# Optimization experiments

Hardware: AMD Instinct MI355X
Metric: run time of the kernel (lower is better)

## Reference

```python
import jax, jax.numpy as jnp
import numpy as np

N = 50000   # nodes
E = 800000  # edges (avg degree 16)
F = 128     # feature dim (input = hidden = output)
H = 8       # heads
D = F // H  # head dim = 16
L = 4       # layers


def setup_inputs() -> dict:
    key = jax.random.key(0)
    ks = jax.random.split(key, 11)
    x = jax.random.normal(ks[0], (N, F), dtype=jnp.float32)
    edge_index = jax.random.randint(ks[1], (2, E), 0, N, dtype=jnp.int64)
    s = 1.0 / np.sqrt(F)
    Wq = jax.random.normal(ks[2], (L, F, F), dtype=jnp.float32) * s
    Wk = jax.random.normal(ks[3], (L, F, F), dtype=jnp.float32) * s
    Wv = jax.random.normal(ks[4], (L, F, F), dtype=jnp.float32) * s
    Ws = jax.random.normal(ks[5], (L, F, F), dtype=jnp.float32) * s  # lin_skip (root weight)
    bq = jax.random.normal(ks[6], (L, F), dtype=jnp.float32) * 0.02
    bk = jax.random.normal(ks[7], (L, F), dtype=jnp.float32) * 0.02
    bv = jax.random.normal(ks[8], (L, F), dtype=jnp.float32) * 0.02
    bs = jax.random.normal(ks[9], (L, F), dtype=jnp.float32) * 0.02
    return {"x": x, "edge_index": edge_index, "Wq": Wq, "bq": bq,
            "Wk": Wk, "bk": bk, "Wv": Wv, "bv": bv, "Ws": Ws, "bs": bs}


def _transformer_conv(x, src, dst, Wq, bq, Wk, bk, Wv, bv, Ws, bs):
    # Q from destination nodes, K/V from source nodes (PyG TransformerConv).
    q = (x @ Wq + bq)[dst].reshape(E, H, D)
    k = (x @ Wk + bk)[src].reshape(E, H, D)
    alpha = (q * k).sum(-1) * (1.0 / np.sqrt(D))            # [E, H]
    # segment softmax over edges grouped by destination node
    amax = jax.ops.segment_max(alpha, dst, num_segments=N)   # [N, H]
    amax = jnp.where(jnp.isfinite(amax), amax, 0.0)
    p = jnp.exp(alpha - amax[dst])
    denom = jax.ops.segment_sum(p, dst, num_segments=N)      # [N, H]
    a = p / denom[dst]                                       # [E, H]
    v = (x @ Wv + bv)[src].reshape(E, H, D)
    msg = (a[..., None] * v).reshape(E, F)
    out = jax.ops.segment_sum(msg, dst, num_segments=N)      # concat heads
    out = out + x @ Ws + bs                                  # root/skip connection
    return out, a


def reference(x, edge_index, Wq, bq, Wk, bk, Wv, bv, Ws, bs):
    src, dst = edge_index[0], edge_index[1]
    alphas = []
    h = x
    for i in range(L - 1):
        h, a = _transformer_conv(h, src, dst, Wq[i], bq[i], Wk[i], bk[i],
                                 Wv[i], bv[i], Ws[i], bs[i])
        h = jax.nn.gelu(h, approximate=False)
        alphas.append(a)
    h, a = _transformer_conv(h, src, dst, Wq[-1], bq[-1], Wk[-1], bk[-1],
                             Wv[-1], bv[-1], Ws[-1], bs[-1])
    alphas.append(a)
    return h, jnp.stack(alphas)  # [N, F], [L, E, H]
```

## Files before the change

kernel.cpp:

```cpp
#include <hip/hip_runtime.h>
#include <math.h>

#define F 128
#define HEADS 8

typedef __attribute__((ext_vector_type(8))) short short8;
typedef __attribute__((ext_vector_type(4))) float floatx4;
typedef __attribute__((ext_vector_type(2))) _Float16 half2v;

__device__ __forceinline__ unsigned short f2bf(float f) {
    unsigned u = __float_as_uint(f);
    unsigned r = u + 0x7FFFu + ((u >> 16) & 1u);
    return (unsigned short)(r >> 16);
}

__device__ __forceinline__ half2v ashalf2(unsigned u) {
    return __builtin_bit_cast(half2v, u);
}
__device__ __forceinline__ unsigned pkh(float a, float b) {
    return __builtin_bit_cast(unsigned, __builtin_amdgcn_cvt_pkrtz(a, b));
}

#if __has_builtin(__builtin_amdgcn_fdot2)
#define FDOT2(a, b, c) __builtin_amdgcn_fdot2((a), (b), (c), false)
#else
#define FDOT2(a, b, c) ((c) + (float)(a)[0] * (float)(b)[0] + (float)(a)[1] * (float)(b)[1])
#endif


__global__ __launch_bounds__(256) void hist_k(const int* __restrict__ dst, int E, int* __restrict__ deg) {
    int e = blockIdx.x * 256 + threadIdx.x;
    if (e < E) atomicAdd(&deg[dst[e]], 1);
}

__global__ __launch_bounds__(256) void scan1_k(const int* __restrict__ deg, int N,
                                               int* __restrict__ start, int* __restrict__ partials) {
    __shared__ int sm[256];
    int t = threadIdx.x;
    int i = blockIdx.x * 256 + t;
    int v = (i < N) ? deg[i] : 0;
    sm[t] = v;
    __syncthreads();
    for (int off = 1; off < 256; off <<= 1) {
        int add = (t >= off) ? sm[t - off] : 0;
        __syncthreads();
        sm[t] += add;
        __syncthreads();
    }
    if (i < N) start[i] = sm[t] - v;
    if (t == 255) partials[blockIdx.x] = sm[t];
}

__global__ __launch_bounds__(256) void scan2_k(int* __restrict__ partials, int nb,
                                               int* __restrict__ start, int N, int E) {
    __shared__ int sm[256];
    int t = threadIdx.x;
    int v = (t < nb) ? partials[t] : 0;
    sm[t] = v;
    __syncthreads();
    for (int off = 1; off < 256; off <<= 1) {
        int add = (t >= off) ? sm[t - off] : 0;
        __syncthreads();
        sm[t] += add;
        __syncthreads();
    }
    if (t < nb) partials[t] = sm[t] - v;
    if (t == 0) start[N] = E;
}

__global__ __launch_bounds__(256) void scan3_k(int* __restrict__ start, int N, const int* __restrict__ partials) {
    int i = blockIdx.x * 256 + threadIdx.x;
    if (i < N) start[i] += partials[blockIdx.x];
}

__global__ __launch_bounds__(256) void fill_k(const int* __restrict__ src, const int* __restrict__ dst, int E,
                                              const int* __restrict__ start, int* __restrict__ cursor,
                                              int2* __restrict__ epair) {
    int e = blockIdx.x * 256 + threadIdx.x;
    if (e < E) {
        int dd = dst[e];
        int pos = atomicAdd(&cursor[dd], 1);
        epair[start[dd] + pos] = make_int2(e, src[e]);
    }
}

__global__ __launch_bounds__(256) void cvt_k(const float* __restrict__ x, unsigned short* __restrict__ xb, int total4) {
    int i = blockIdx.x * 256 + threadIdx.x;
    if (i < total4) {
        float4 v = ((const float4*)x)[i];
        ushort4 o;
        o.x = f2bf(v.x); o.y = f2bf(v.y); o.z = f2bf(v.z); o.w = f2bf(v.w);
        ((ushort4*)xb)[i] = o;
    }
}


__global__ __launch_bounds__(256) void wprep_k(
    const float* __restrict__ Wq, const float* __restrict__ Wk,
    const float* __restrict__ Wv, const float* __restrict__ Ws,
    unsigned short* __restrict__ out, int total) {
    int idx = blockIdx.x * 256 + threadIdx.x;
    if (idx >= total) return;
    int j = idx & 7;
    int lane = (idx >> 3) & 63;
    int rest = idx >> 9;
    int chunk = rest & 3;
    int ftile = (rest >> 2) & 7;
    int mat = (rest >> 5) & 3;
    int layer = rest >> 7;
    int k = chunk * 32 + (lane >> 4) * 8 + j;
    int f = ftile * 16 + (lane & 15);
    const float* W = (mat == 0) ? Wq : (mat == 1) ? Wk : (mat == 2) ? Wv : Ws;
    out[idx] = f2bf(W[((size_t)layer * F + k) * F + f]);
}


__global__ __launch_bounds__(256) void gemm_mfma(
    const unsigned short* __restrict__ xb, const unsigned short* __restrict__ wfrag,
    const float* __restrict__ bq, const float* __restrict__ bk,
    const float* __restrict__ bv, const float* __restrict__ bs,
    unsigned short* __restrict__ Qh, unsigned short* __restrict__ Kh,
    unsigned short* __restrict__ Vh, float* __restrict__ S, int N) {
    int wave = threadIdx.x >> 6;
    int lane = threadIdx.x & 63;
    int row0 = blockIdx.x * 32;
    int lm = lane & 15, quad = lane >> 4;
    const unsigned short* wf = wfrag + wave * 16384;

    floatx4 acc[2][8];
#pragma unroll
    for (int t = 0; t < 2; t++)
#pragma unroll
        for (int u = 0; u < 8; u++) acc[t][u] = (floatx4){0.f, 0.f, 0.f, 0.f};

#pragma unroll
    for (int chunk = 0; chunk < 4; chunk++) {
        short8 xfr[2];
#pragma unroll
        for (int t = 0; t < 2; t++) {
            int m = row0 + t * 16 + lm;
            m = (m < N) ? m : (N - 1);
            xfr[t] = *(const short8*)(xb + (size_t)m * F + chunk * 32 + quad * 8);
        }
#pragma unroll
        for (int u = 0; u < 8; u++) {
            short8 wfr = *(const short8*)(wf + ((u * 4 + chunk) * 64 + lane) * 8);
            acc[0][u] = __builtin_amdgcn_mfma_f32_16x16x32_bf16(wfr, xfr[0], acc[0][u], 0, 0, 0);
            acc[1][u] = __builtin_amdgcn_mfma_f32_16x16x32_bf16(wfr, xfr[1], acc[1][u], 0, 0, 0);
        }
    }

    const float* bias = (wave == 0) ? bq : (wave == 1) ? bk : (wave == 2) ? bv : bs;
#pragma unroll
    for (int u = 0; u < 8; u++) {
        float4 bv4 = *(const float4*)&bias[u * 16 + quad * 4];
#pragma unroll
        for (int t = 0; t < 2; t++) {
            int node = row0 + t * 16 + lm;
            if (node < N) {
                floatx4 a = acc[t][u];
                size_t off = (size_t)node * F + u * 16 + quad * 4;
                float v0 = a[0] + bv4.x, v1 = a[1] + bv4.y, v2 = a[2] + bv4.z, v3 = a[3] + bv4.w;
                if (wave == 3) {
                    *(float4*)&S[off] = make_float4(v0, v1, v2, v3);
                } else {
                    unsigned short* dp = (wave == 0) ? Qh : (wave == 1) ? Kh : Vh;
                    *(uint2*)&dp[off] = make_uint2(pkh(v0, v1), pkh(v2, v3));
                }
            }
        }
    }
}


__device__ __forceinline__ float gelu_exact(float v) {
    return 0.5f * v * (1.0f + erff(v * 0.70710678118654752f));
}

__global__ __launch_bounds__(256) void edge_k(
    const unsigned short* __restrict__ Qh, const unsigned short* __restrict__ Kh,
    const unsigned short* __restrict__ Vh, const float* __restrict__ S,
    const int* __restrict__ start, const int2* __restrict__ epair,
    float* __restrict__ aout,
    float* __restrict__ hout_f, unsigned short* __restrict__ hout_b,
    int N, int do_gelu) {
    __shared__ float wbuf[4][64][8];
    __shared__ int sbuf[4][64];
    __shared__ int ebuf[4][64];
    __shared__ float mdbuf[4][8];

    int wv = threadIdx.x >> 6;
    int lane = threadIdx.x & 63;
    int n = blockIdx.x * 4 + wv;
    if (n >= N) return;

    int beg = start[n], end = start[n + 1];
    int deg = end - beg;
    bool multi = deg > 64;
    int slot = lane >> 3, h = lane & 7;
    int g = lane >> 4, fl = lane & 15;
    int fh = fl >> 1;

    const unsigned short* qp = Qh + (size_t)n * F + h * 16;
    uint4 qa = *(const uint4*)(qp);
    uint4 qc = *(const uint4*)(qp + 8);
    half2v q0 = ashalf2(qa.x), q1 = ashalf2(qa.y), q2 = ashalf2(qa.z), q3 = ashalf2(qa.w);
    half2v q4 = ashalf2(qc.x), q5 = ashalf2(qc.y), q6 = ashalf2(qc.z), q7 = ashalf2(qc.w);

    float d = 0.f;
    float a0 = 0.f, a1 = 0.f, a2 = 0.f, a3 = 0.f, a4 = 0.f, a5 = 0.f, a6 = 0.f, a7 = 0.f;

    for (int c0 = beg; c0 < end; c0 += 64) {
        int cnt = min(64, end - c0);

        int nit = (cnt + 7) >> 3;
        for (int it = 0; it < nit; it++) {
            int idx = it * 8 + slot;
            bool val = idx < cnt;
            int gi = c0 + (val ? idx : 0);
            int2 pe = epair[gi];
            int s = pe.y;
            const unsigned short* kp = Kh + (size_t)s * F + h * 16;
            uint4 ka = *(const uint4*)(kp);
            uint4 kc = *(const uint4*)(kp + 8);
            float p0 = 0.f, p1 = 0.f;
            p0 = FDOT2(q0, ashalf2(ka.x), p0);
            p0 = FDOT2(q1, ashalf2(ka.y), p0);
            p0 = FDOT2(q2, ashalf2(ka.z), p0);
            p0 = FDOT2(q3, ashalf2(ka.w), p0);
            p1 = FDOT2(q4, ashalf2(kc.x), p1);
            p1 = FDOT2(q5, ashalf2(kc.y), p1);
            p1 = FDOT2(q6, ashalf2(kc.z), p1);
            p1 = FDOT2(q7, ashalf2(kc.w), p1);
            float w = __expf((p0 + p1) * 0.25f);
            if (!val) w = 0.f;
            d += w;
            wbuf[wv][idx][h] = w;
            if (h == 0) { sbuf[wv][idx] = s; ebuf[wv][idx] = pe.x; }
            if (multi && val) aout[(size_t)pe.x * HEADS + h] = w;
        }

        for (int j = 0; j < cnt; j += 8) {
            int idx0 = j + g;
            int idx1 = j + 4 + g;
            bool v0 = idx0 < cnt;
            bool v1 = idx1 < cnt;
            int s0 = sbuf[wv][v0 ? idx0 : 0];
            int s1 = sbuf[wv][v1 ? idx1 : 0];
            float w0 = wbuf[wv][v0 ? idx0 : 0][fh];
            float w1 = wbuf[wv][v1 ? idx1 : 0][fh];
            if (!v0) w0 = 0.f;
            if (!v1) w1 = 0.f;
            uint4 va = *(const uint4*)&Vh[(size_t)s0 * F + fl * 8];
            uint4 vb2 = *(const uint4*)&Vh[(size_t)s1 * F + fl * 8];
            half2v x0 = ashalf2(va.x), x1 = ashalf2(va.y), x2 = ashalf2(va.z), x3 = ashalf2(va.w);
            half2v y0 = ashalf2(vb2.x), y1 = ashalf2(vb2.y), y2 = ashalf2(vb2.z), y3 = ashalf2(vb2.w);
            a0 += w0 * (float)x0[0]; a1 += w0 * (float)x0[1];
            a2 += w0 * (float)x1[0]; a3 += w0 * (float)x1[1];
            a4 += w0 * (float)x2[0]; a5 += w0 * (float)x2[1];
            a6 += w0 * (float)x3[0]; a7 += w0 * (float)x3[1];
            a0 += w1 * (float)y0[0]; a1 += w1 * (float)y0[1];
            a2 += w1 * (float)y1[0]; a3 += w1 * (float)y1[1];
            a4 += w1 * (float)y2[0]; a5 += w1 * (float)y2[1];
            a6 += w1 * (float)y3[0]; a7 += w1 * (float)y3[1];
        }
    }

    d += __shfl_xor(d, 8);
    d += __shfl_xor(d, 16);
    d += __shfl_xor(d, 32);
    float inv_d = (d > 0.f) ? 1.f / d : 0.f;
    if (slot == 0) mdbuf[wv][h] = inv_d;

    if (!multi) {
        for (int idx = slot; idx < deg; idx += 8)
            aout[(size_t)ebuf[wv][idx] * HEADS + h] = wbuf[wv][idx][h] * inv_d;
    } else {
        for (int idx = slot; idx < deg; idx += 8)
            aout[(size_t)epair[beg + idx].x * HEADS + h] *= inv_d;
    }

    a0 += __shfl_xor(a0, 16); a0 += __shfl_xor(a0, 32);
    a1 += __shfl_xor(a1, 16); a1 += __shfl_xor(a1, 32);
    a2 += __shfl_xor(a2, 16); a2 += __shfl_xor(a2, 32);
    a3 += __shfl_xor(a3, 16); a3 += __shfl_xor(a3, 32);
    a4 += __shfl_xor(a4, 16); a4 += __shfl_xor(a4, 32);
    a5 += __shfl_xor(a5, 16); a5 += __shfl_xor(a5, 32);
    a6 += __shfl_xor(a6, 16); a6 += __shfl_xor(a6, 32);
    a7 += __shfl_xor(a7, 16); a7 += __shfl_xor(a7, 32);

    if (lane < 16) {
        float invd = mdbuf[wv][fh];
        const float* sp = S + (size_t)n * F + fl * 8;
        float4 s0 = *(const float4*)(sp + 0);
        float4 s1 = *(const float4*)(sp + 4);
        float o0 = a0 * invd + s0.x, o1 = a1 * invd + s0.y;
        float o2 = a2 * invd + s0.z, o3 = a3 * invd + s0.w;
        float o4 = a4 * invd + s1.x, o5 = a5 * invd + s1.y;
        float o6 = a6 * invd + s1.z, o7 = a7 * invd + s1.w;
        if (do_gelu) {
            o0 = gelu_exact(o0); o1 = gelu_exact(o1); o2 = gelu_exact(o2); o3 = gelu_exact(o3);
            o4 = gelu_exact(o4); o5 = gelu_exact(o5); o6 = gelu_exact(o6); o7 = gelu_exact(o7);
            uint4 ob;
            ob.x = (unsigned)f2bf(o0) | ((unsigned)f2bf(o1) << 16);
            ob.y = (unsigned)f2bf(o2) | ((unsigned)f2bf(o3) << 16);
            ob.z = (unsigned)f2bf(o4) | ((unsigned)f2bf(o5) << 16);
            ob.w = (unsigned)f2bf(o6) | ((unsigned)f2bf(o7) << 16);
            *(uint4*)&hout_b[(size_t)n * F + fl * 8] = ob;
        } else {
            float* op = hout_f + (size_t)n * F + fl * 8;
            *(float4*)(op + 0) = make_float4(o0, o1, o2, o3);
            *(float4*)(op + 4) = make_float4(o4, o5, o6, o7);
        }
    }
}


extern "C" void kernel_launch(void* const* d_in, const int* in_sizes, int n_in,
                              void* d_out, int out_size, void* d_ws, size_t ws_size,
                              hipStream_t stream) {
    const float* x  = (const float*)d_in[0];
    const int*   ei = (const int*)d_in[1];
    const float* Wq = (const float*)d_in[2];
    const float* bq = (const float*)d_in[3];
    const float* Wk = (const float*)d_in[4];
    const float* bk = (const float*)d_in[5];
    const float* Wv = (const float*)d_in[6];
    const float* bv = (const float*)d_in[7];
    const float* Ws = (const float*)d_in[8];
    const float* bs = (const float*)d_in[9];

    const int N = in_sizes[0] / F;
    const int E = in_sizes[1] / 2;
    const int L = in_sizes[2] / (F * F);

    float* Sb = (float*)d_ws;
    unsigned short* Qh = (unsigned short*)(Sb + (size_t)N * F);
    unsigned short* xb = Qh + (size_t)N * F;
    unsigned short* hb = xb + (size_t)N * F;
    unsigned short* Kb = hb + (size_t)N * F;
    unsigned short* Vb = Kb + (size_t)N * F;
    unsigned short* wfrag = Vb + (size_t)N * F;
    int2* epair = (int2*)(wfrag + (size_t)L * 4 * 16384);
    int* start = (int*)(epair + E);
    int* cursor = start + (N + 1);
    int* partials = cursor + N;

    float* out_h = (float*)d_out;
    float* out_a = out_h + (size_t)N * F;

    const int* srcIdx = ei;
    const int* dstIdx = ei + E;

    int nbScan = (N + 255) / 256;
    hipMemsetAsync(cursor, 0, sizeof(int) * N, stream);
    hist_k<<<(E + 255) / 256, 256, 0, stream>>>(dstIdx, E, cursor);
    scan1_k<<<nbScan, 256, 0, stream>>>(cursor, N, start, partials);
    scan2_k<<<1, 256, 0, stream>>>(partials, nbScan, start, N, E);
    scan3_k<<<nbScan, 256, 0, stream>>>(start, N, partials);
    hipMemsetAsync(cursor, 0, sizeof(int) * N, stream);
    fill_k<<<(E + 255) / 256, 256, 0, stream>>>(srcIdx, dstIdx, E, start, cursor, epair);

    int wtotal = L * 4 * 16384;
    wprep_k<<<(wtotal + 255) / 256, 256, 0, stream>>>(Wq, Wk, Wv, Ws, wfrag, wtotal);
    cvt_k<<<((N * F / 4) + 255) / 256, 256, 0, stream>>>(x, xb, N * F / 4);

    for (int l = 0; l < L; ++l) {
        const unsigned short* hin = (l == 0) ? xb : hb;
        gemm_mfma<<<(N + 31) / 32, 256, 0, stream>>>(
            hin, wfrag + (size_t)l * 4 * 16384,
            bq + (size_t)l * F, bk + (size_t)l * F,
            bv + (size_t)l * F, bs + (size_t)l * F,
            Qh, Kb, Vb, Sb, N);
        edge_k<<<(N + 3) / 4, 256, 0, stream>>>(
            Qh, Kb, Vb, Sb, start, epair,
            out_a + (size_t)l * E * HEADS, out_h, hb, N, (l < L - 1) ? 1 : 0);
    }
}
```

Measured before the change: 685.8 us.

## Load edge pairs once per chunk into registers and software-prefetch K/V gathers

Each lane now loads one (edge id, source) pair per 64-edge chunk, and the indices are broadcast with wave shuffles instead of being staged through shared sbuf/ebuf arrays. The K-row gather for the next iteration and the V-row gathers for the next step are issued before the current dot products and accumulations, a register double-buffering scheme meant to hide gather latency. This raises register pressure, and the clamped prefetch indices cause some redundant loads at chunk tails.

```diff
diff --git a/kernel.cpp b/kernel.cpp
--- a/kernel.cpp
+++ b/kernel.cpp
@@ -185,8 +185,6 @@
     float* __restrict__ hout_f, unsigned short* __restrict__ hout_b,
     int N, int do_gelu) {
     __shared__ float wbuf[4][64][8];
-    __shared__ int sbuf[4][64];
-    __shared__ int ebuf[4][64];
     __shared__ float mdbuf[4][8];
 
     int wv = threadIdx.x >> 6;
@@ -209,20 +207,32 @@
 
     float d = 0.f;
     float a0 = 0.f, a1 = 0.f, a2 = 0.f, a3 = 0.f, a4 = 0.f, a5 = 0.f, a6 = 0.f, a7 = 0.f;
+    int2 peL = make_int2(0, 0);
 
     for (int c0 = beg; c0 < end; c0 += 64) {
         int cnt = min(64, end - c0);
 
+        int2 pe = epair[c0 + min(lane, cnt - 1)];
+        peL = pe;
+
+        int s0 = __shfl(pe.y, g, 64);
+        int s1 = __shfl(pe.y, 4 + g, 64);
+        uint4 va = *(const uint4*)&Vh[(size_t)s0 * F + fl * 8];
+        uint4 vb2 = *(const uint4*)&Vh[(size_t)s1 * F + fl * 8];
+
         int nit = (cnt + 7) >> 3;
+        int idx = slot;
+        int s = __shfl(pe.y, idx, 64);
+        const unsigned short* kp = Kh + (size_t)s * F + h * 16;
+        uint4 ka = *(const uint4*)kp;
+        uint4 kc = *(const uint4*)(kp + 8);
         for (int it = 0; it < nit; it++) {
-            int idx = it * 8 + slot;
+            int nidx = idx + 8;
+            int ns = __shfl(pe.y, min(nidx, 63), 64);
+            const unsigned short* nkp = Kh + (size_t)ns * F + h * 16;
+            uint4 nka = *(const uint4*)nkp;
+            uint4 nkc = *(const uint4*)(nkp + 8);
             bool val = idx < cnt;
-            int gi = c0 + (val ? idx : 0);
-            int2 pe = epair[gi];
-            int s = pe.y;
-            const unsigned short* kp = Kh + (size_t)s * F + h * 16;
-            uint4 ka = *(const uint4*)(kp);
-            uint4 kc = *(const uint4*)(kp + 8);
             float p0 = 0.f, p1 = 0.f;
             p0 = FDOT2(q0, ashalf2(ka.x), p0);
             p0 = FDOT2(q1, ashalf2(ka.y), p0);
@@ -236,23 +246,22 @@
             if (!val) w = 0.f;
             d += w;
             wbuf[wv][idx][h] = w;
-            if (h == 0) { sbuf[wv][idx] = s; ebuf[wv][idx] = pe.x; }
-            if (multi && val) aout[(size_t)pe.x * HEADS + h] = w;
+            if (multi) {
+                int eid = __shfl(pe.x, idx, 64);
+                if (val) aout[(size_t)eid * HEADS + h] = w;
+            }
+            ka = nka; kc = nkc; idx = nidx;
         }
 
         for (int j = 0; j < cnt; j += 8) {
-            int idx0 = j + g;
-            int idx1 = j + 4 + g;
-            bool v0 = idx0 < cnt;
-            bool v1 = idx1 < cnt;
-            int s0 = sbuf[wv][v0 ? idx0 : 0];
-            int s1 = sbuf[wv][v1 ? idx1 : 0];
-            float w0 = wbuf[wv][v0 ? idx0 : 0][fh];
-            float w1 = wbuf[wv][v1 ? idx1 : 0][fh];
-            if (!v0) w0 = 0.f;
-            if (!v1) w1 = 0.f;
-            uint4 va = *(const uint4*)&Vh[(size_t)s0 * F + fl * 8];
-            uint4 vb2 = *(const uint4*)&Vh[(size_t)s1 * F + fl * 8];
+            int ns0 = __shfl(pe.y, min(j + 8 + g, 63), 64);
+            int ns1 = __shfl(pe.y, min(j + 12 + g, 63), 64);
+            uint4 na = *(const uint4*)&Vh[(size_t)ns0 * F + fl * 8];
+            uint4 nb = *(const uint4*)&Vh[(size_t)ns1 * F + fl * 8];
+            bool v0 = (j + g) < cnt;
+            bool v1 = (j + 4 + g) < cnt;
+            float w0 = v0 ? wbuf[wv][j + g][fh] : 0.f;
+            float w1 = v1 ? wbuf[wv][j + 4 + g][fh] : 0.f;
             half2v x0 = ashalf2(va.x), x1 = ashalf2(va.y), x2 = ashalf2(va.z), x3 = ashalf2(va.w);
             half2v y0 = ashalf2(vb2.x), y1 = ashalf2(vb2.y), y2 = ashalf2(vb2.z), y3 = ashalf2(vb2.w);
             a0 += w0 * (float)x0[0]; a1 += w0 * (float)x0[1];
@@ -263,6 +272,7 @@
             a2 += w1 * (float)y1[0]; a3 += w1 * (float)y1[1];
             a4 += w1 * (float)y2[0]; a5 += w1 * (float)y2[1];
             a6 += w1 * (float)y3[0]; a7 += w1 * (float)y3[1];
+            va = na; vb2 = nb;
         }
     }
 
@@ -273,8 +283,11 @@
     if (slot == 0) mdbuf[wv][h] = inv_d;
 
     if (!multi) {
-        for (int idx = slot; idx < deg; idx += 8)
-            aout[(size_t)ebuf[wv][idx] * HEADS + h] = wbuf[wv][idx][h] * inv_d;
+        for (int base = 0; base < deg; base += 8) {
+            int idx = base + slot;
+            int eid = __shfl(peL.x, min(idx, 63), 64);
+            if (idx < deg) aout[(size_t)eid * HEADS + h] = wbuf[wv][idx][h] * inv_d;
+        }
     } else {
         for (int idx = slot; idx < deg; idx += 8)
             aout[(size_t)epair[beg + idx].x * HEADS + h] *= inv_d;
@@ -292,12 +305,12 @@
     if (lane < 16) {
         float invd = mdbuf[wv][fh];
         const float* sp = S + (size_t)n * F + fl * 8;
-        float4 s0 = *(const float4*)(sp + 0);
-        float4 s1 = *(const float4*)(sp + 4);
-        float o0 = a0 * invd + s0.x, o1 = a1 * invd + s0.y;
-        float o2 = a2 * invd + s0.z, o3 = a3 * invd + s0.w;
-        float o4 = a4 * invd + s1.x, o5 = a5 * invd + s1.y;
-        float o6 = a6 * invd + s1.z, o7 = a7 * invd + s1.w;
+        float4 s0v = *(const float4*)(sp + 0);
+        float4 s1v = *(const float4*)(sp + 4);
+        float o0 = a0 * invd + s0v.x, o1 = a1 * invd + s0v.y;
+        float o2 = a2 * invd + s0v.z, o3 = a3 * invd + s0v.w;
+        float o4 = a4 * invd + s1v.x, o5 = a5 * invd + s1v.y;
+        float o6 = a6 * invd + s1v.z, o7 = a7 * invd + s1v.w;
         if (do_gelu) {
             o0 = gelu_exact(o0); o1 = gelu_exact(o1); o2 = gelu_exact(o2); o3 = gelu_exact(o3);
             o4 = gelu_exact(o4); o5 = gelu_exact(o5); o6 = gelu_exact(o6); o7 = gelu_exact(o7);
```

After: 703.8 us. 2.6% more time.
